# Kernel optimization log

Measured on AMD Instinct MI355X. Metric: run time of the kernel, lower is better.

Reference implementation:

```python
import jax, jax.numpy as jnp
import numpy as np

EPS = 1e-7
MAX_TANGENT_NORM = 1.5
SCALE = 16.0 / 8.0  # alpha / rank


def _exp_map_zero(vs, K, max_norm):
    # vs: [..., n] spatial tangent at origin (time component is 0).
    # Returns (x0, xs): Lorentz point time/spatial parts, <x,x>_L = -1/K.
    sqrtK = jnp.sqrt(K)
    n = jnp.linalg.norm(vs, axis=-1, keepdims=True)
    nc = jnp.minimum(n, max_norm)                       # clamp tangent norm (TB-PAG)
    vs_c = vs * (nc / jnp.maximum(n, EPS))
    t = sqrtK * nc
    x0 = jnp.cosh(t) / sqrtK
    xs = jnp.sinh(t) / (sqrtK * jnp.maximum(nc, EPS)) * vs_c
    return x0, xs


def _log_map_zero_spatial(x0, xs, K):
    # Inverse of exp at origin; returns spatial part of tangent vector.
    sqrtK = jnp.sqrt(K)
    d = jnp.arccosh(jnp.maximum(sqrtK * x0, 1.0 + EPS)) / sqrtK  # geodesic distance
    ns = jnp.linalg.norm(xs, axis=-1, keepdims=True)
    return d * xs / jnp.maximum(ns, EPS)


def setup_inputs() -> dict:
    key = jax.random.key(0)
    k1, k2, k3, k4, k5 = jax.random.split(key, 5)
    Bsz, S, D, R = 4, 2048, 4096, 8
    x = jax.random.normal(k1, (Bsz, S, D), dtype=jnp.float32)
    W = jax.random.normal(k2, (D, D), dtype=jnp.float32) * (1.0 / np.sqrt(D))
    b = jax.random.normal(k3, (D,), dtype=jnp.float32) * 0.01
    A = jax.random.normal(k4, (D, R), dtype=jnp.float32) * 0.01
    B = jax.random.normal(k5, (R, D), dtype=jnp.float32) * 0.01
    log_K = jnp.zeros((), dtype=jnp.float32)  # K = 1.0
    return {"x": x, "W": W, "b": b, "A": A, "B": B, "log_K": log_K}


def reference(x, W, b, A, B, log_K):
    K = jnp.clip(jnp.exp(log_K), 1e-4, 10.0)
    # frozen Euclidean base: z = x @ W^T + b
    z_base = jnp.einsum('bsd,od->bso', x, W) + b
    # project Euclidean hidden state onto H^n: exp_map_zero([0, x])
    x0, xs = _exp_map_zero(x, K, MAX_TANGENT_NORM)
    # LLR: tangent vector at origin, rank-r bottleneck, back to manifold
    v = _log_map_zero_spatial(x0, xs, K)            # [b,s,d]
    v_adapted = (v @ A) @ B                          # rank-8 bottleneck
    y0, ys = _exp_map_zero(v_adapted, K, MAX_TANGENT_NORM)
    # project back to Euclidean (spatial slice of log map)
    delta = _log_map_zero_spatial(y0, ys, K)
    return z_base + delta * SCALE
```

## Files before the change

kernel.cpp:

```cpp
#include <hip/hip_runtime.h>
#include <hip/hip_bf16.h>


#define DD 4096
#define MR 8192
#define BM 256
#define BN 256
#define BK 64

typedef float f32x4 __attribute__((ext_vector_type(4)));
typedef __bf16 bf16x8 __attribute__((ext_vector_type(8)));

#define GLOAD_LDS16(gptr, lptr)                                                        \
  __builtin_amdgcn_global_load_lds((const __attribute__((address_space(1))) void*)(gptr), \
                                   (__attribute__((address_space(3))) void*)(lptr), 16, 0, 0)

__device__ __forceinline__ __bf16 f2bf(float f) { return (__bf16)f; }

__global__ __launch_bounds__(256) void k_prep(const float* __restrict__ x,
                                              const float* __restrict__ W,
                                              const float* __restrict__ A,
                                              const float* __restrict__ Bm,
                                              __bf16* __restrict__ Xb,
                                              __bf16* __restrict__ Wb,
                                              float* __restrict__ U,
                                              float* __restrict__ G) {
  int bid = blockIdx.x;
  int t = threadIdx.x;
  int lane = t & 63, wid = t >> 6;

  if (bid == 0) {
    float g[64];
#pragma unroll
    for (int i = 0; i < 64; ++i) g[i] = 0.f;
    for (int d = t; d < DD; d += 256) {
      float br[8];
#pragma unroll
      for (int r = 0; r < 8; ++r) br[r] = Bm[r * DD + d];
#pragma unroll
      for (int r = 0; r < 8; ++r)
#pragma unroll
        for (int s = 0; s < 8; ++s) g[r * 8 + s] += br[r] * br[s];
    }
    __shared__ float gs[4][64];
#pragma unroll
    for (int i = 0; i < 64; ++i) {
      float v = g[i];
      for (int off = 32; off >= 1; off >>= 1) v += __shfl_down(v, off, 64);
      if (lane == 0) gs[wid][i] = v;
    }
    __syncthreads();
    if (t < 64) G[t] = gs[0][t] + gs[1][t] + gs[2][t] + gs[3][t];
  } else if (bid <= 8192) {
    int row = bid - 1;
    const float* xr = x + (size_t)row * DD;
    __bf16* xbr = Xb + (size_t)row * DD;
    float nsq = 0.f;
    float p[8] = {0, 0, 0, 0, 0, 0, 0, 0};
#pragma unroll
    for (int i = 0; i < 16; ++i) {
      int d = t + 256 * i;
      float xv = xr[d];
      xbr[d] = f2bf(xv);
      nsq += xv * xv;
      f32x4 a0 = *reinterpret_cast<const f32x4*>(A + (size_t)d * 8);
      f32x4 a1 = *reinterpret_cast<const f32x4*>(A + (size_t)d * 8 + 4);
      p[0] += xv * a0[0]; p[1] += xv * a0[1]; p[2] += xv * a0[2]; p[3] += xv * a0[3];
      p[4] += xv * a1[0]; p[5] += xv * a1[1]; p[6] += xv * a1[2]; p[7] += xv * a1[3];
    }
    for (int off = 32; off >= 1; off >>= 1) {
      nsq += __shfl_down(nsq, off, 64);
#pragma unroll
      for (int r = 0; r < 8; ++r) p[r] += __shfl_down(p[r], off, 64);
    }
    __shared__ float red[4][9];
    if (lane == 0) {
      red[wid][0] = nsq;
#pragma unroll
      for (int r = 0; r < 8; ++r) red[wid][1 + r] = p[r];
    }
    __syncthreads();
    if (t == 0) {
      float ns = red[0][0] + red[1][0] + red[2][0] + red[3][0];
      float u[8];
#pragma unroll
      for (int r = 0; r < 8; ++r)
        u[r] = red[0][1 + r] + red[1][1 + r] + red[2][1 + r] + red[3][1 + r];
      float n = sqrtf(ns);
      float s1 = fminf(n, 1.5f) / fmaxf(n, 1e-7f);
#pragma unroll
      for (int r = 0; r < 8; ++r) U[(size_t)row * 8 + r] = s1 * u[r];
    }
  } else {
    int i = (bid - 8193) * 256 + t;
    const f32x4* s = reinterpret_cast<const f32x4*>(W) + (size_t)i * 2;
    f32x4 v0 = s[0], v1 = s[1];
    bf16x8 o;
    o[0] = f2bf(v0[0]); o[1] = f2bf(v0[1]); o[2] = f2bf(v0[2]); o[3] = f2bf(v0[3]);
    o[4] = f2bf(v1[0]); o[5] = f2bf(v1[1]); o[6] = f2bf(v1[2]); o[7] = f2bf(v1[3]);
    reinterpret_cast<bf16x8*>(Wb)[i] = o;
  }
}

__global__ __launch_bounds__(512, 2) void k_gemm(const __bf16* __restrict__ Xb,
                                                 const __bf16* __restrict__ Wb,
                                                 const float* __restrict__ bias,
                                                 const float* __restrict__ U,
                                                 const float* __restrict__ G,
                                                 const float* __restrict__ Bm,
                                                 float* __restrict__ out) {
  __shared__ union {
    char raw[131072];
    struct { float cs[256][8]; float bs2[8][256]; } epi;
  } sm;
  char* smc = sm.raw;

  const int nwg = (MR / BM) * (DD / BN);
  int wg = ((int)blockIdx.x % 8) * (nwg / 8) + (int)blockIdx.x / 8;
  int tm = wg / (DD / BN);
  int tn = wg % (DD / BN);
  int row0 = tm * BM, col0 = tn * BN;

  int t = threadIdx.x;
  int lane = t & 63, wid = t >> 6;
  int wm = wid >> 2, wn = wid & 3;
  int fr = lane & 15;
  int hi = lane >> 4;
  int sw = (fr >> 1) & 3;

  f32x4 acc[8][4] = {};
  bf16x8 aF[4], bF[4];

  auto STAGE = [&](const __bf16* mat, int rowbase, int tau, int ks, int ldsOff) {
    int j = (t & 3) ^ ((t >> 3) & 3);
    int kk = ((tau & 63) << 6) + (ks << 5) + (j << 3);
    const __bf16* src = mat + (size_t)(rowbase + (t >> 2)) * DD + kk;
    char* dst = smc + ldsOff + t * 16;
    GLOAD_LDS16(src, dst);
    GLOAD_LDS16(src + (size_t)128 * DD, dst + 8192);
  };

#define LDA(buf, ks, mbase)                                                     \
  _Pragma("unroll") for (int j = 0; j < 4; ++j) aF[j] =                         \
      *reinterpret_cast<const bf16x8*>(smc + (buf)*65536 + 16384 + (ks)*32768 + \
                                       (wm * 128 + ((mbase) + j) * 16 + fr) * 64 + \
                                       ((hi ^ sw) << 4));
#define LDB(buf, ks)                                                            \
  _Pragma("unroll") for (int j = 0; j < 4; ++j) bF[j] =                         \
      *reinterpret_cast<const bf16x8*>(smc + (buf)*65536 + (ks)*32768 +         \
                                       (wn * 64 + j * 16 + fr) * 64 +           \
                                       ((hi ^ sw) << 4));
#define MMQ(mbase)                                                              \
  __builtin_amdgcn_s_setprio(1);                                                \
  _Pragma("unroll") for (int j = 0; j < 4; ++j)                                 \
      _Pragma("unroll") for (int n = 0; n < 4; ++n)                             \
          acc[(mbase) + j][n] = __builtin_amdgcn_mfma_f32_16x16x32_bf16(        \
              aF[j], bF[n], acc[(mbase) + j][n], 0, 0, 0);                      \
  __builtin_amdgcn_s_setprio(0);
#define BAR() __builtin_amdgcn_s_barrier()
#define LGKM0() asm volatile("s_waitcnt lgkmcnt(0)" ::: "memory")

  STAGE(Wb, col0, 0, 0, 0);
  STAGE(Xb, row0, 0, 0, 16384);
  STAGE(Wb, col0, 0, 1, 32768);
  STAGE(Xb, row0, 0, 1, 49152);
  asm volatile("s_waitcnt vmcnt(4)" ::: "memory");
  STAGE(Wb, col0, 1, 0, 65536 + 0);
  STAGE(Xb, row0, 1, 0, 65536 + 16384);
  STAGE(Wb, col0, 1, 1, 65536 + 32768);
  asm volatile("s_waitcnt vmcnt(6)" ::: "memory");
  BAR();

  for (int i = 0; i < DD / BK / 2; ++i) {
    int T = 2 * i;
    LDA(0, 0, 0); LDB(0, 0);
    STAGE(Xb, row0, T + 1, 1, 65536 + 49152);
    BAR(); LGKM0();
    MMQ(0);
    BAR();
    LDA(0, 0, 4);
    STAGE(Wb, col0, T + 2, 0, 0);
    BAR(); LGKM0();
    MMQ(4);
    BAR();
    LDA(0, 1, 0); LDB(0, 1);
    STAGE(Xb, row0, T + 2, 0, 16384);
    BAR(); LGKM0();
    MMQ(0);
    BAR();
    LDA(0, 1, 4);
    STAGE(Wb, col0, T + 2, 1, 32768);
    BAR(); LGKM0();
    MMQ(4);
    asm volatile("s_waitcnt vmcnt(6)" ::: "memory");
    BAR();
    LDA(1, 0, 0); LDB(1, 0);
    STAGE(Xb, row0, T + 2, 1, 49152);
    BAR(); LGKM0();
    MMQ(0);
    BAR();
    LDA(1, 0, 4);
    STAGE(Wb, col0, T + 3, 0, 65536 + 0);
    BAR(); LGKM0();
    MMQ(4);
    BAR();
    LDA(1, 1, 0); LDB(1, 1);
    STAGE(Xb, row0, T + 3, 0, 65536 + 16384);
    BAR(); LGKM0();
    MMQ(0);
    BAR();
    LDA(1, 1, 4);
    STAGE(Wb, col0, T + 3, 1, 65536 + 32768);
    BAR(); LGKM0();
    MMQ(4);
    asm volatile("s_waitcnt vmcnt(6)" ::: "memory");
    BAR();
  }

  asm volatile("s_waitcnt vmcnt(0)" ::: "memory");
  __syncthreads();
  {
    int rr = t >> 6, cc = (t & 63) * 4;
    *reinterpret_cast<f32x4*>(&sm.epi.bs2[rr][cc]) =
        *reinterpret_cast<const f32x4*>(Bm + (size_t)rr * DD + col0 + cc);
  }
  if (t < 256) {
    f32x4 u0 = *reinterpret_cast<const f32x4*>(U + (size_t)(row0 + t) * 8);
    f32x4 u1 = *reinterpret_cast<const f32x4*>(U + (size_t)(row0 + t) * 8 + 4);
    float u[8] = {u0[0], u0[1], u0[2], u0[3], u1[0], u1[1], u1[2], u1[3]};
    float n2sq = 0.f;
#pragma unroll
    for (int r = 0; r < 8; ++r) {
      float s = 0.f;
#pragma unroll
      for (int q = 0; q < 8; ++q) s += G[r * 8 + q] * u[q];
      n2sq += u[r] * s;
    }
    float n2 = sqrtf(fmaxf(n2sq, 0.f));
    float sc2 = 2.0f * fminf(n2, 1.5f) / fmaxf(n2, 1e-7f);
#pragma unroll
    for (int r = 0; r < 8; ++r) sm.epi.cs[t][r] = sc2 * u[r];
  }
  __syncthreads();

  int colb = col0 + wn * 64 + fr;
  float biasv[4], bcol[4][8];
#pragma unroll
  for (int n = 0; n < 4; ++n) {
    biasv[n] = bias[colb + n * 16];
#pragma unroll
    for (int r = 0; r < 8; ++r) bcol[n][r] = sm.epi.bs2[r][wn * 64 + fr + n * 16];
  }
#pragma unroll
  for (int m = 0; m < 8; ++m) {
#pragma unroll
    for (int j = 0; j < 4; ++j) {
      int rl = wm * 128 + m * 16 + hi * 4 + j;
      float c0 = sm.epi.cs[rl][0], c1 = sm.epi.cs[rl][1], c2 = sm.epi.cs[rl][2],
            c3 = sm.epi.cs[rl][3], c4 = sm.epi.cs[rl][4], c5 = sm.epi.cs[rl][5],
            c6 = sm.epi.cs[rl][6], c7 = sm.epi.cs[rl][7];
      float* orow = out + (size_t)(row0 + rl) * DD + colb;
#pragma unroll
      for (int n = 0; n < 4; ++n) {
        float delta = c0 * bcol[n][0] + c1 * bcol[n][1] + c2 * bcol[n][2] +
                      c3 * bcol[n][3] + c4 * bcol[n][4] + c5 * bcol[n][5] +
                      c6 * bcol[n][6] + c7 * bcol[n][7];
        orow[n * 16] = acc[m][n][j] + biasv[n] + delta;
      }
    }
  }
}

extern "C" void kernel_launch(void* const* d_in, const int* in_sizes, int n_in,
                              void* d_out, int out_size, void* d_ws, size_t ws_size,
                              hipStream_t stream) {
  const float* x = (const float*)d_in[0];
  const float* W = (const float*)d_in[1];
  const float* b = (const float*)d_in[2];
  const float* A = (const float*)d_in[3];
  const float* Bm = (const float*)d_in[4];
  float* out = (float*)d_out;

  char* ws = (char*)d_ws;
  __bf16* Xb = (__bf16*)ws;
  __bf16* Wb = (__bf16*)(ws + (size_t)64 * 1024 * 1024);
  float* U = (float*)(ws + (size_t)96 * 1024 * 1024);
  float* G = (float*)(ws + (size_t)96 * 1024 * 1024 + 256 * 1024);

  k_prep<<<1 + 8192 + 8192, 256, 0, stream>>>(x, W, A, Bm, Xb, Wb, U, G);
  k_gemm<<<(MR / BM) * (DD / BN), 512, 0, stream>>>(Xb, Wb, b, U, G, Bm, out);
}
```

Baseline: 359.6 us.

## Double-buffer MFMA register fragments and vectorize prep-kernel row loads

The GEMM main loop now keeps two sets of A/B register fragments. LDS reads for the next quarter-step are issued before the current MFMA block runs, and the explicit lgkmcnt(0) waits are dropped, so LDS latency can overlap with matrix math. Separately, the prep kernel loads each row with contiguous float4 reads and writes the bf16 copy as 16-byte vectors instead of strided scalar accesses. The cost is more register pressure from the extra fragments. Ordering correctness now depends on compiler-inserted waits and the existing barriers, which is a risk with the global_load_lds writes near the final stage.

```diff
diff --git a/kernel.cpp b/kernel.cpp
--- a/kernel.cpp
+++ b/kernel.cpp
@@ -55,19 +55,34 @@
     int row = bid - 1;
     const float* xr = x + (size_t)row * DD;
     __bf16* xbr = Xb + (size_t)row * DD;
+    int base = t << 4;
+    f32x4 xv[4];
+#pragma unroll
+    for (int q = 0; q < 4; ++q)
+      xv[q] = *reinterpret_cast<const f32x4*>(xr + base + q * 4);
     float nsq = 0.f;
     float p[8] = {0, 0, 0, 0, 0, 0, 0, 0};
 #pragma unroll
-    for (int i = 0; i < 16; ++i) {
-      int d = t + 256 * i;
-      float xv = xr[d];
-      xbr[d] = f2bf(xv);
-      nsq += xv * xv;
-      f32x4 a0 = *reinterpret_cast<const f32x4*>(A + (size_t)d * 8);
-      f32x4 a1 = *reinterpret_cast<const f32x4*>(A + (size_t)d * 8 + 4);
-      p[0] += xv * a0[0]; p[1] += xv * a0[1]; p[2] += xv * a0[2]; p[3] += xv * a0[3];
-      p[4] += xv * a1[0]; p[5] += xv * a1[1]; p[6] += xv * a1[2]; p[7] += xv * a1[3];
-    }
+    for (int q = 0; q < 4; ++q)
+#pragma unroll
+      for (int j = 0; j < 4; ++j) {
+        float x1 = xv[q][j];
+        nsq += x1 * x1;
+        int d = base + q * 4 + j;
+        f32x4 a0 = *reinterpret_cast<const f32x4*>(A + (size_t)d * 8);
+        f32x4 a1 = *reinterpret_cast<const f32x4*>(A + (size_t)d * 8 + 4);
+        p[0] += x1 * a0[0]; p[1] += x1 * a0[1]; p[2] += x1 * a0[2]; p[3] += x1 * a0[3];
+        p[4] += x1 * a1[0]; p[5] += x1 * a1[1]; p[6] += x1 * a1[2]; p[7] += x1 * a1[3];
+      }
+    bf16x8 o0, o1;
+#pragma unroll
+    for (int j = 0; j < 4; ++j) {
+      o0[j] = f2bf(xv[0][j]); o0[4 + j] = f2bf(xv[1][j]);
+      o1[j] = f2bf(xv[2][j]); o1[4 + j] = f2bf(xv[3][j]);
+    }
+    *reinterpret_cast<bf16x8*>(xbr + base) = o0;
+    *reinterpret_cast<bf16x8*>(xbr + base + 8) = o1;
+
     for (int off = 32; off >= 1; off >>= 1) {
       nsq += __shfl_down(nsq, off, 64);
 #pragma unroll
@@ -129,7 +144,7 @@
   int sw = (fr >> 1) & 3;
 
   f32x4 acc[8][4] = {};
-  bf16x8 aF[4], bF[4];
+  bf16x8 aA[4], aB[4], bA[4], bB[4];
 
   auto STAGE = [&](const __bf16* mat, int rowbase, int tau, int ks, int ldsOff) {
     int j = (t & 3) ^ ((t >> 3) & 3);
@@ -140,25 +155,25 @@
     GLOAD_LDS16(src + (size_t)128 * DD, dst + 8192);
   };
 
-#define LDA(buf, ks, mbase)                                                     \
-  _Pragma("unroll") for (int j = 0; j < 4; ++j) aF[j] =                         \
+#define LDA(dst, buf, ks, mbase)                                                \
+  _Pragma("unroll") for (int j = 0; j < 4; ++j) dst[j] =                        \
       *reinterpret_cast<const bf16x8*>(smc + (buf)*65536 + 16384 + (ks)*32768 + \
                                        (wm * 128 + ((mbase) + j) * 16 + fr) * 64 + \
                                        ((hi ^ sw) << 4));
-#define LDB(buf, ks)                                                            \
-  _Pragma("unroll") for (int j = 0; j < 4; ++j) bF[j] =                         \
+#define LDB(dst, buf, ks)                                                       \
+  _Pragma("unroll") for (int j = 0; j < 4; ++j) dst[j] =                        \
       *reinterpret_cast<const bf16x8*>(smc + (buf)*65536 + (ks)*32768 +         \
                                        (wn * 64 + j * 16 + fr) * 64 +           \
                                        ((hi ^ sw) << 4));
-#define MMQ(mbase)                                                              \
+#define MMQ(aset, bset, mbase)                                                  \
   __builtin_amdgcn_s_setprio(1);                                                \
   _Pragma("unroll") for (int j = 0; j < 4; ++j)                                 \
       _Pragma("unroll") for (int n = 0; n < 4; ++n)                             \
           acc[(mbase) + j][n] = __builtin_amdgcn_mfma_f32_16x16x32_bf16(        \
-              aF[j], bF[n], acc[(mbase) + j][n], 0, 0, 0);                      \
+              aset[j], bset[n], acc[(mbase) + j][n], 0, 0, 0);                  \
   __builtin_amdgcn_s_setprio(0);
 #define BAR() __builtin_amdgcn_s_barrier()
-#define LGKM0() asm volatile("s_waitcnt lgkmcnt(0)" ::: "memory")
+#define VM6() asm volatile("s_waitcnt vmcnt(6)" ::: "memory")
 
   STAGE(Wb, col0, 0, 0, 0);
   STAGE(Xb, row0, 0, 0, 16384);
@@ -168,52 +183,58 @@
   STAGE(Wb, col0, 1, 0, 65536 + 0);
   STAGE(Xb, row0, 1, 0, 65536 + 16384);
   STAGE(Wb, col0, 1, 1, 65536 + 32768);
-  asm volatile("s_waitcnt vmcnt(6)" ::: "memory");
+  VM6();
   BAR();
+  LDA(aA, 0, 0, 0);
+  LDB(bA, 0, 0);
 
   for (int i = 0; i < DD / BK / 2; ++i) {
     int T = 2 * i;
-    LDA(0, 0, 0); LDB(0, 0);
     STAGE(Xb, row0, T + 1, 1, 65536 + 49152);
-    BAR(); LGKM0();
-    MMQ(0);
-    BAR();
-    LDA(0, 0, 4);
+    BAR();
+    LDA(aB, 0, 0, 4);
+    MMQ(aA, bA, 0);
+    BAR();
     STAGE(Wb, col0, T + 2, 0, 0);
-    BAR(); LGKM0();
-    MMQ(4);
-    BAR();
-    LDA(0, 1, 0); LDB(0, 1);
+    BAR();
+    LDA(aA, 0, 1, 0);
+    LDB(bB, 0, 1);
+    MMQ(aB, bA, 4);
+    BAR();
     STAGE(Xb, row0, T + 2, 0, 16384);
-    BAR(); LGKM0();
-    MMQ(0);
-    BAR();
-    LDA(0, 1, 4);
+    BAR();
+    LDA(aB, 0, 1, 4);
+    MMQ(aA, bB, 0);
+    BAR();
     STAGE(Wb, col0, T + 2, 1, 32768);
-    BAR(); LGKM0();
-    MMQ(4);
-    asm volatile("s_waitcnt vmcnt(6)" ::: "memory");
-    BAR();
-    LDA(1, 0, 0); LDB(1, 0);
+    BAR();
+    VM6();
+    LDA(aA, 1, 0, 0);
+    LDB(bA, 1, 0);
+    MMQ(aB, bB, 4);
+    BAR();
     STAGE(Xb, row0, T + 2, 1, 49152);
-    BAR(); LGKM0();
-    MMQ(0);
-    BAR();
-    LDA(1, 0, 4);
+    BAR();
+    LDA(aB, 1, 0, 4);
+    MMQ(aA, bA, 0);
+    BAR();
     STAGE(Wb, col0, T + 3, 0, 65536 + 0);
-    BAR(); LGKM0();
-    MMQ(4);
-    BAR();
-    LDA(1, 1, 0); LDB(1, 1);
+    BAR();
+    LDA(aA, 1, 1, 0);
+    LDB(bB, 1, 1);
+    MMQ(aB, bA, 4);
+    BAR();
     STAGE(Xb, row0, T + 3, 0, 65536 + 16384);
-    BAR(); LGKM0();
-    MMQ(0);
-    BAR();
-    LDA(1, 1, 4);
+    BAR();
+    LDA(aB, 1, 1, 4);
+    MMQ(aA, bB, 0);
+    BAR();
     STAGE(Wb, col0, T + 3, 1, 65536 + 32768);
-    BAR(); LGKM0();
-    MMQ(4);
-    asm volatile("s_waitcnt vmcnt(6)" ::: "memory");
+    BAR();
+    VM6();
+    LDA(aA, 0, 0, 0);
+    LDB(bA, 0, 0);
+    MMQ(aB, bB, 4);
     BAR();
   }
 
```

Result: slower. 410.6 us (+14.2%).
